# Performance work log

Hardware: AMD Instinct MI355X
Metric: run time of the kernel (lower is better)

## Reference

```python
import jax, jax.numpy as jnp
import numpy as np

B, T, W, R, N = 32, 256, 128, 4, 128
IFACE = R * W + 3 * W + 5 * R + 3   # 919
INSZ = (R + 1) * W                  # 640
DELTA = 1e-6

def _lstm_step(x, h, c, Wih, Whh, bih, bhh):
    g = x @ Wih.T + bih + h @ Whh.T + bhh
    i, f, gg, o = jnp.split(g, 4, axis=-1)
    c = jax.nn.sigmoid(f) * c + jax.nn.sigmoid(i) * jnp.tanh(gg)
    return jax.nn.sigmoid(o) * jnp.tanh(c), c

def _cosine(mem, keys):
    # mem [b,n,w], keys [b,h,w] -> [b,h,n]
    mn = mem / (jnp.linalg.norm(mem, axis=2, keepdims=True) + DELTA)
    kn = keys / (jnp.linalg.norm(keys, axis=2, keepdims=True) + DELTA)
    return jnp.einsum('bhw,bnw->bhn', kn, mn)

def _memory_step(xi, st):
    # xi: [b, IFACE] interface vector; st: DNC memory state
    mem, link, prec, rw, ww, usage = st
    b = xi.shape[0]
    o1 = R * W; o2 = o1 + R; o3 = o2 + W; o4 = o3 + 1
    o5 = o4 + W; o6 = o5 + W; o7 = o6 + R; o8 = o7 + 1; o9 = o8 + 1
    read_keys = jnp.tanh(xi[:, :o1].reshape(b, R, W))
    read_str = jax.nn.softplus(xi[:, o1:o2])
    write_key = jnp.tanh(xi[:, o2:o3])
    write_str = jax.nn.softplus(xi[:, o3:o4])
    erase = jax.nn.sigmoid(xi[:, o4:o5])
    write_vec = jnp.tanh(xi[:, o5:o6])
    free_gates = jax.nn.sigmoid(xi[:, o6:o7])
    alloc_gate = jax.nn.sigmoid(xi[:, o7:o8])
    write_gate = jax.nn.sigmoid(xi[:, o8:o9])
    read_modes = jax.nn.softmax(xi[:, o9:].reshape(b, R, 3), axis=-1)
    # usage vector update (single write head)
    usage = usage + (1 - usage) * ww
    usage = usage * jnp.prod(1 - free_gates[:, :, None] * rw, axis=1)
    # write content weighting [b,n]
    wc = jax.nn.softmax(_cosine(mem, write_key[:, None, :])[:, 0, :] * write_str, axis=1)
    # allocation weighting: sort ascending, exclusive cumprod, unsort
    u = DELTA + (1 - DELTA) * usage
    phi = jnp.argsort(u, axis=1)
    su = jnp.take_along_axis(u, phi, axis=1)
    prod_su = jnp.cumprod(jnp.concatenate([jnp.ones((b, 1), u.dtype), su], axis=1), axis=1)[:, :-1]
    alloc = jnp.take_along_axis((1 - su) * prod_su, jnp.argsort(phi, axis=1), axis=1)
    # write weighting [b,n]
    ww = write_gate * (alloc_gate * alloc + (1 - alloc_gate) * wc)
    # erase then write
    mem = mem * (1 - ww[:, :, None] * erase[:, None, :]) + ww[:, :, None] * write_vec[:, None, :]
    # temporal link matrix [b,n,n], zero diagonal
    link = (1 - ww[:, :, None] - ww[:, None, :]) * link + ww[:, :, None] * prec[:, None, :]
    link = link * (1 - jnp.eye(N, dtype=link.dtype))
    prec = (1 - jnp.sum(ww, axis=1, keepdims=True)) * prec + ww
    # read weighting: content + forward/backward temporal modes
    rc = jax.nn.softmax(_cosine(mem, read_keys) * read_str[:, :, None], axis=2)
    fw = jnp.einsum('bij,brj->bri', link, rw)
    bw = jnp.einsum('brj,bji->bri', rw, link)
    rw = read_modes[:, :, 0:1] * bw + read_modes[:, :, 1:2] * fw + read_modes[:, :, 2:3] * rc
    read_vecs = jnp.einsum('brn,bnw->bwr', rw, mem)  # [b,w,r] as used by controller
    return read_vecs, (mem, link, prec, rw, ww, usage)

def _forward(input, enc_Wih, enc_Whh, enc_bih, enc_bhh, ctl_Wih, ctl_Whh, ctl_bih, ctl_bhh, iface_W, iface_b, out_W, out_b):
    dt = input.dtype
    h0 = jnp.zeros((B, W), dt)
    def enc_step(carry, x_t):
        h, c = _lstm_step(x_t, carry[0], carry[1], enc_Wih, enc_Whh, enc_bih, enc_bhh)
        return (h, c), h
    _, enc = jax.lax.scan(enc_step, (h0, h0), jnp.swapaxes(input, 0, 1))  # enc: [T,B,W]
    z = lambda *s: jnp.zeros(s, dt)
    mem0 = (z(B, N, W), z(B, N, N), z(B, N), z(B, R, N), z(B, N), z(B, N))
    def step(carry, enc_t):
        h, c, rv, mst = carry
        # cat([b,w,1],[b,w,r]) then flatten -> interleaved per memory-cell element, as in torch
        x = jnp.concatenate([enc_t[:, :, None], rv], axis=2).reshape(B, INSZ)
        h, c = _lstm_step(x, h, c, ctl_Wih, ctl_Whh, ctl_bih, ctl_bhh)
        xi = h @ iface_W.T + iface_b
        rv, mst = _memory_step(xi, mst)
        out_t = jnp.concatenate([h, rv.reshape(B, W * R)], axis=1) @ out_W.T + out_b
        return (h, c, rv, mst), out_t
    _, outs = jax.lax.scan(step, (h0, h0, z(B, W, R), mem0), enc)
    return jnp.swapaxes(outs, 0, 1)  # [B,T,W]

def setup_inputs():
    key = jax.random.key(0)
    ks = jax.random.split(key, 8)
    p = lambda k, s: jax.random.normal(k, s, jnp.float32) * 0.05
    return {
        'input': jax.random.normal(ks[0], (B, T, W), jnp.float32),
        'source_lengths': jnp.full((B,), T, jnp.int32),
        'enc_Wih': p(ks[1], (4 * W, W)), 'enc_Whh': p(ks[2], (4 * W, W)),
        'enc_bih': jnp.zeros((4 * W,), jnp.float32), 'enc_bhh': jnp.zeros((4 * W,), jnp.float32),
        'ctl_Wih': p(ks[3], (4 * W, INSZ)), 'ctl_Whh': p(ks[4], (4 * W, W)),
        'ctl_bih': jnp.zeros((4 * W,), jnp.float32), 'ctl_bhh': jnp.zeros((4 * W,), jnp.float32),
        'iface_W': p(ks[5], (IFACE, W)), 'iface_b': jnp.zeros((IFACE,), jnp.float32),
        'out_W': p(ks[6], (W, INSZ)), 'out_b': jnp.zeros((W,), jnp.float32),
    }

def reference(input, source_lengths, enc_Wih, enc_Whh, enc_bih, enc_bhh, ctl_Wih, ctl_Whh, ctl_bih, ctl_bhh, iface_W, iface_b, out_W, out_b):
    # source_lengths are all == T (full-length sequences), so pack/pad is identity.
    return _forward(input, enc_Wih, enc_Whh, enc_bih, enc_bhh, ctl_Wih, ctl_Whh, ctl_bih, ctl_bhh, iface_W, iface_b, out_W, out_b)
```

## Files before the change

### kernel.cpp

```cpp
#include <hip/hip_runtime.h>

typedef unsigned short u16;
typedef unsigned int u32;

#define NT 1024
#define Bv 32
#define Tv 256
#define Wv 128
#define Rv 4
#define Nv 128
#define DELTAv 1e-6f

__device__ __forceinline__ float bf2f(u16 u){
  union { u32 i; float f; } c; c.i = ((u32)u) << 16; return c.f;
}
__device__ __forceinline__ u16 f2bf(float f){
  union { float f; u32 u; } c; c.f = f;
  u32 u = c.u;
  return (u16)((u + 0x7fffu + ((u >> 16) & 1u)) >> 16);
}
__device__ __forceinline__ void unp(u32 v, float& a, float& b){
  union { u32 i; float f; } c0, c1;
  c0.i = v << 16; c1.i = v & 0xffff0000u;
  a = c0.f; b = c1.f;
}
__device__ __forceinline__ float sigm(float x){ return 1.0f / (1.0f + __expf(-x)); }
__device__ __forceinline__ float softplusf(float x){ return fmaxf(x, 0.f) + log1pf(__expf(-fabsf(x))); }
__device__ __forceinline__ float wredsum(float v){
  #pragma unroll
  for (int o = 32; o > 0; o >>= 1) v += __shfl_down(v, o, 64);
  return v;
}
__device__ __forceinline__ float wredmax(float v){
  #pragma unroll
  for (int o = 32; o > 0; o >>= 1) v = fmaxf(v, __shfl_down(v, o, 64));
  return v;
}
__device__ __forceinline__ float ldval(const void* p, int idx, int dt32){
  return dt32 ? ((const float*)p)[idx] : bf2f(((const u16*)p)[idx]);
}

__global__ void detect_dtype(const u16* __restrict__ buf, int* __restrict__ flag){
  int lane = threadIdx.x;
  float crazy = 0.f;
  for (int i = 0; i < 4; i++){
    u16 v = buf[lane * 4 + i];
    int e = (v >> 7) & 0xFF;
    if (e != 0 && (e < 117 || e > 137)) crazy += 1.f;
  }
  crazy = wredsum(crazy);
  if (lane == 0) flag[0] = (crazy >= 32.f) ? 1 : 0;
}

__global__ void pack_w(const void* __restrict__ src, u32* __restrict__ dst,
                       int Js, int Jd, int K, const int* __restrict__ flag){
  int j = blockIdx.x * 256 + threadIdx.x;
  int k2 = blockIdx.y;
  if (j >= Jd) return;
  u16 lo = 0, hi = 0;
  if (j < Js){
    if (flag[0]){
      const float* s = (const float*)src;
      lo = f2bf(s[(size_t)j * K + 2 * k2]);
      hi = f2bf(s[(size_t)j * K + 2 * k2 + 1]);
    } else {
      const u16* s = (const u16*)src;
      lo = s[(size_t)j * K + 2 * k2];
      hi = s[(size_t)j * K + 2 * k2 + 1];
    }
  }
  dst[(size_t)k2 * Jd + j] = (u32)lo | ((u32)hi << 16);
}

__device__ __forceinline__ int permctl(int c){
  if (c < 128) return 5 * c;
  int q = c - 128; return 5 * (q & 127) + 1 + (q >> 7);
}
__device__ __forceinline__ int permout(int c){
  if (c < 128) return c;
  int q = c - 128; return 128 + 4 * (q & 127) + (q >> 7);
}

__global__ void pack_ctl(const void* __restrict__ src, u32* __restrict__ dst,
                         const int* __restrict__ flag){
  int j = blockIdx.x * 256 + threadIdx.x;
  int k2 = blockIdx.y;
  if (j >= 512) return;
  int c0 = permctl(2 * k2), c1 = permctl(2 * k2 + 1);
  u16 lo, hi;
  if (flag[0]){
    const float* s = (const float*)src;
    lo = f2bf(s[(size_t)j * 640 + c0]); hi = f2bf(s[(size_t)j * 640 + c1]);
  } else {
    const u16* s = (const u16*)src;
    lo = s[(size_t)j * 640 + c0]; hi = s[(size_t)j * 640 + c1];
  }
  dst[(size_t)k2 * 512 + j] = (u32)lo | ((u32)hi << 16);
}

__global__ void pack_out(const void* __restrict__ src, u32* __restrict__ dst,
                         const int* __restrict__ flag){
  int j = threadIdx.x;
  int k2 = blockIdx.y;
  if (j >= 128) return;
  int c0 = permout(2 * k2), c1 = permout(2 * k2 + 1);
  u16 lo, hi;
  if (flag[0]){
    const float* s = (const float*)src;
    lo = f2bf(s[(size_t)j * 640 + c0]); hi = f2bf(s[(size_t)j * 640 + c1]);
  } else {
    const u16* s = (const u16*)src;
    lo = s[(size_t)j * 640 + c0]; hi = s[(size_t)j * 640 + c1];
  }
  dst[(size_t)k2 * 128 + j] = (u32)lo | ((u32)hi << 16);
}

__global__ void fill_half(u16* __restrict__ p, int n){
  int i = blockIdx.x * 256 + threadIdx.x;
  if (i < n) p[i] = 0x3F00;
}

__global__ __launch_bounds__(NT) void dnc_main(
    const void* __restrict__ input,
    const void* __restrict__ enc_bih_g, const void* __restrict__ enc_bhh_g,
    const void* __restrict__ ctl_bih_g, const void* __restrict__ ctl_bhh_g,
    const void* __restrict__ iface_b_g, const void* __restrict__ out_b_g,
    const u32* __restrict__ encPW, const u32* __restrict__ ctlPW,
    const u32* __restrict__ ifPW, const u32* __restrict__ outPW,
    void* __restrict__ outp, const int* __restrict__ dtflag)
{
  const int bid = blockIdx.x;
  const int tid = threadIdx.x;
  const int lane = tid & 63;
  const int wid = tid >> 6;
  const int dt32 = dtflag[0];

  __shared__ __align__(16) float memS[Nv * 129];
  __shared__ __align__(16) float linkS[Nv * 129];
  __shared__ __align__(16) float pp[NT];
  __shared__ __align__(16) float ppE[512];
  __shared__ __align__(16) float xhC[768];
  __shared__ __align__(16) float xinS[128];
  __shared__ __align__(16) float rkeyS[512], rwS[512], rcS[512];
  __shared__ __align__(16) float wkeyS[128], eraseS[128], wvecS[128];
  __shared__ __align__(16) float wwS[128], usageS[128], precS[128], wcS[128];
  __shared__ __align__(16) float uS[128], sortedU[128], scanA[128];
  __shared__ __align__(16) float encBias[512], ctlBias[512];
  __shared__ __align__(16) float outBias[128];
  __shared__ float rstrS[4], fgS[4], rmRaw[12], rmS[12], scal[8];

  const int wE = (tid >= 919) ? (tid - 919) : (tid < 23 ? 105 + tid : -1);
  float cE = 0.f;
  float cC = 0.f;

  if (tid < 512){
    encBias[tid] = ldval(enc_bih_g, tid, dt32) + ldval(enc_bhh_g, tid, dt32);
    ctlBias[tid] = ldval(ctl_bih_g, tid, dt32) + ldval(ctl_bhh_g, tid, dt32);
    rwS[tid] = 0.f;
  }
  if (tid < 768) xhC[tid] = 0.f;
  if (tid < 128){
    outBias[tid] = ldval(out_b_g, tid, dt32);
    wwS[tid] = 0.f; usageS[tid] = 0.f; precS[tid] = 0.f;
  }
  for (int i = tid; i < Nv * 129; i += NT){ memS[i] = 0.f; linkS[i] = 0.f; }
  if (tid < 64){
    int idx = (bid * Tv + 0) * Wv + 2 * tid;
    xinS[2 * tid] = ldval(input, idx, dt32);
    xinS[2 * tid + 1] = ldval(input, idx + 1, dt32);
  }
  __syncthreads();

  if (tid >= 512){
    int o = tid - 512;
    const u32* wp = encPW + o;
    float a0 = 0.f, a1 = 0.f;
    #pragma unroll 8
    for (int k2 = 0; k2 < 64; k2++){
      float w0, w1; unp(wp[k2 * 512], w0, w1);
      float2 x2 = *(const float2*)(xinS + 2 * k2);
      a0 = fmaf(x2.x, w0, a0); a1 = fmaf(x2.y, w1, a1);
    }
    ppE[o] = a0 + a1;
  }
  __syncthreads();
  if (wE >= 0){
    float g0 = ppE[wE] + encBias[wE];
    float g1 = ppE[128 + wE] + encBias[128 + wE];
    float g2 = ppE[256 + wE] + encBias[256 + wE];
    float g3 = ppE[384 + wE] + encBias[384 + wE];
    float cn = sigm(g1) * cE + sigm(g0) * tanhf(g2);
    cE = cn;
    xhC[wE] = sigm(g3) * tanhf(cn);
  }
  if (tid >= 64 && tid < 128){
    int w2 = (tid - 64) * 2;
    int idx = (bid * Tv + 1) * Wv + w2;
    xinS[w2] = ldval(input, idx, dt32);
    xinS[w2 + 1] = ldval(input, idx + 1, dt32);
  }
  __syncthreads();

  for (int t = 0; t < Tv; ++t){
    {
      int o = tid & 511, s = tid >> 9;
      const u32* wp = ctlPW + (s * 192) * 512 + o;
      const float* xp = xhC + s * 384;
      float a0 = 0.f, a1 = 0.f;
      u32 wb[8];
      #pragma unroll
      for (int i = 0; i < 8; i++) wb[i] = wp[i * 512];
      #pragma unroll 1
      for (int c = 0; c < 184; c += 8){
        u32 wn[8];
        #pragma unroll
        for (int i = 0; i < 8; i++) wn[i] = wp[(c + 8 + i) * 512];
        #pragma unroll
        for (int i = 0; i < 8; i++){
          float w0, w1; unp(wb[i], w0, w1);
          float2 x2 = *(const float2*)(xp + 2 * (c + i));
          a0 = fmaf(x2.x, w0, a0); a1 = fmaf(x2.y, w1, a1);
          wb[i] = wn[i];
        }
      }
      #pragma unroll
      for (int i = 0; i < 8; i++){
        float w0, w1; unp(wb[i], w0, w1);
        float2 x2 = *(const float2*)(xp + 2 * (184 + i));
        a0 = fmaf(x2.x, w0, a0); a1 = fmaf(x2.y, w1, a1);
      }
      pp[tid] = a0 + a1;
    }
    __syncthreads();

    if (tid < 128){
      float g0 = pp[tid] + pp[512 + tid] + ctlBias[tid];
      float g1 = pp[128 + tid] + pp[640 + tid] + ctlBias[128 + tid];
      float g2 = pp[256 + tid] + pp[768 + tid] + ctlBias[256 + tid];
      float g3 = pp[384 + tid] + pp[896 + tid] + ctlBias[384 + tid];
      float cn = sigm(g1) * cC + sigm(g0) * tanhf(g2);
      cC = cn;
      xhC[640 + tid] = sigm(g3) * tanhf(cn);
    } else if (tid >= 512){
      int o = tid - 512;
      const u32* wp = encPW + o;
      float a0 = 0.f, a1 = 0.f;
      u32 wb[8];
      #pragma unroll
      for (int i = 0; i < 8; i++) wb[i] = wp[i * 512];
      #pragma unroll 1
      for (int c = 0; c < 56; c += 8){
        u32 wn[8];
        #pragma unroll
        for (int i = 0; i < 8; i++) wn[i] = wp[(c + 8 + i) * 512];
        #pragma unroll
        for (int i = 0; i < 8; i++){
          float w0, w1; unp(wb[i], w0, w1);
          float2 x2 = *(const float2*)(xinS + 2 * (c + i));
          a0 = fmaf(x2.x, w0, a0); a1 = fmaf(x2.y, w1, a1);
          wb[i] = wn[i];
        }
      }
      #pragma unroll
      for (int i = 0; i < 8; i++){
        float w0, w1; unp(wb[i], w0, w1);
        float2 x2 = *(const float2*)(xinS + 2 * (56 + i));
        a0 = fmaf(x2.x, w0, a0); a1 = fmaf(x2.y, w1, a1);
      }
      const u32* wq = encPW + 64 * 512 + o;
      #pragma unroll
      for (int i = 0; i < 8; i++) wb[i] = wq[i * 512];
      #pragma unroll 1
      for (int c = 0; c < 56; c += 8){
        u32 wn[8];
        #pragma unroll
        for (int i = 0; i < 8; i++) wn[i] = wq[(c + 8 + i) * 512];
        #pragma unroll
        for (int i = 0; i < 8; i++){
          float w0, w1; unp(wb[i], w0, w1);
          float2 x2 = *(const float2*)(xhC + 2 * (c + i));
          a0 = fmaf(x2.x, w0, a0); a1 = fmaf(x2.y, w1, a1);
          wb[i] = wn[i];
        }
      }
      #pragma unroll
      for (int i = 0; i < 8; i++){
        float w0, w1; unp(wb[i], w0, w1);
        float2 x2 = *(const float2*)(xhC + 2 * (56 + i));
        a0 = fmaf(x2.x, w0, a0); a1 = fmaf(x2.y, w1, a1);
      }
      ppE[o] = a0 + a1;
    }
    __syncthreads();

    if (tid < 919){
      const u32* wp = ifPW + tid;
      const float* xp = xhC + 640;
      float a0 = ldval(iface_b_g, tid, dt32), a1 = 0.f;
      u32 wb[8];
      #pragma unroll
      for (int i = 0; i < 8; i++) wb[i] = wp[i * 928];
      #pragma unroll 1
      for (int c = 0; c < 56; c += 8){
        u32 wn[8];
        #pragma unroll
        for (int i = 0; i < 8; i++) wn[i] = wp[(c + 8 + i) * 928];
        #pragma unroll
        for (int i = 0; i < 8; i++){
          float w0, w1; unp(wb[i], w0, w1);
          float2 x2 = *(const float2*)(xp + 2 * (c + i));
          a0 = fmaf(x2.x, w0, a0); a1 = fmaf(x2.y, w1, a1);
          wb[i] = wn[i];
        }
      }
      #pragma unroll
      for (int i = 0; i < 8; i++){
        float w0, w1; unp(wb[i], w0, w1);
        float2 x2 = *(const float2*)(xp + 2 * (56 + i));
        a0 = fmaf(x2.x, w0, a0); a1 = fmaf(x2.y, w1, a1);
      }
      pp[tid] = a0 + a1;
    }
    if (wE >= 0){
      float g0 = ppE[wE] + encBias[wE];
      float g1 = ppE[128 + wE] + encBias[128 + wE];
      float g2 = ppE[256 + wE] + encBias[256 + wE];
      float g3 = ppE[384 + wE] + encBias[384 + wE];
      float cn = sigm(g1) * cE + sigm(g0) * tanhf(g2);
      cE = cn;
      xhC[wE] = sigm(g3) * tanhf(cn);
    }
    __syncthreads();

    if (tid < 919){
      float v = pp[tid];
      if (tid < 512) rkeyS[tid] = tanhf(v);
      else if (tid < 516) rstrS[tid - 512] = softplusf(v);
      else if (tid < 644) wkeyS[tid - 516] = tanhf(v);
      else if (tid == 644) scal[0] = softplusf(v);
      else if (tid < 773) eraseS[tid - 645] = sigm(v);
      else if (tid < 901) wvecS[tid - 773] = tanhf(v);
      else if (tid < 905) fgS[tid - 901] = sigm(v);
      else if (tid == 905) scal[1] = sigm(v);
      else if (tid == 906) scal[2] = sigm(v);
      else rmRaw[tid - 907] = v;
    } else if (tid >= 928 && tid < 992){
      int w2 = (tid - 928) * 2;
      int col = (t + 2 < Tv) ? t + 2 : Tv - 1;
      int idx = (bid * Tv + col) * Wv + w2;
      xinS[w2] = ldval(input, idx, dt32);
      xinS[w2 + 1] = ldval(input, idx + 1, dt32);
    }
    __syncthreads();

    if (wid < 5){
      float* arr = (wid < 4) ? (rkeyS + wid * 128) : wkeyS;
      float a = arr[lane], bq = arr[lane + 64];
      float s = wredsum(a * a + bq * bq);
      s = __shfl(s, 0, 64);
      float inv = 1.0f / (sqrtf(s) + DELTAv);
      arr[lane] = a * inv; arr[lane + 64] = bq * inv;
    } else if (wid < 7){
      int n = (wid - 5) * 64 + lane;
      float us = usageS[n];
      us = us + (1.f - us) * wwS[n];
      float ret = (1.f - fgS[0] * rwS[n]) * (1.f - fgS[1] * rwS[128 + n]) *
                  (1.f - fgS[2] * rwS[256 + n]) * (1.f - fgS[3] * rwS[384 + n]);
      usageS[n] = us * ret;
    } else if (tid >= 448 && tid < 452){
      int r = tid - 448;
      float m0 = rmRaw[3 * r], m1 = rmRaw[3 * r + 1], m2 = rmRaw[3 * r + 2];
      float mx = fmaxf(m0, fmaxf(m1, m2));
      float e0 = __expf(m0 - mx), e1 = __expf(m1 - mx), e2 = __expf(m2 - mx);
      float s = e0 + e1 + e2;
      rmS[3 * r] = e0 / s; rmS[3 * r + 1] = e1 / s; rmS[3 * r + 2] = e2 / s;
    }
    __syncthreads();

    if (tid < 128){
      float sq = 0.f, dt = 0.f;
      #pragma unroll 8
      for (int j = 0; j < 128; j++){
        float m = memS[tid * 129 + j];
        sq = fmaf(m, m, sq); dt = fmaf(m, wkeyS[j], dt);
      }
      wcS[tid] = dt / (sqrtf(sq) + DELTAv) * scal[0];
    } else if (tid < 256){
      uS[tid - 128] = DELTAv + (1.f - DELTAv) * usageS[tid - 128];
    }
    __syncthreads();

    int rnk = 0;
    if (wid == 0){
      float a = wcS[lane], bq = wcS[lane + 64];
      float mx = wredmax(fmaxf(a, bq)); mx = __shfl(mx, 0, 64);
      float ea = __expf(a - mx), eb = __expf(bq - mx);
      float s = wredsum(ea + eb); s = __shfl(s, 0, 64);
      wcS[lane] = ea / s; wcS[lane + 64] = eb / s;
    } else if (tid >= 64 && tid < 192){
      int n = tid - 64;
      float un = uS[n];
      int r = 0;
      for (int m = 0; m < 128; m++){
        float um = uS[m];
        r += (um < un) || (um == un && m < n);
      }
      rnk = r;
      sortedU[r] = un;
    }
    __syncthreads();

    if (wid == 8){
      float a = sortedU[2 * lane], bq = sortedU[2 * lane + 1];
      float p = a * bq;
      float incl = p;
      #pragma unroll
      for (int o = 1; o < 64; o <<= 1){
        float tv = __shfl_up(incl, o, 64);
        if (lane >= o) incl *= tv;
      }
      float ex = __shfl_up(incl, 1, 64);
      if (lane == 0) ex = 1.f;
      scanA[2 * lane] = ex * a;
      scanA[2 * lane + 1] = ex * p;
    }
    __syncthreads();

    if (tid >= 64 && tid < 192){
      int n = tid - 64;
      float ex = (rnk == 0) ? 1.f : scanA[rnk - 1];
      float al = (1.f - uS[n]) * ex;
      wwS[n] = scal[2] * (scal[1] * al + (1.f - scal[1]) * wcS[n]);
    }
    __syncthreads();

    if (wid == 0){
      float s = wredsum(wwS[lane] + wwS[64 + lane]);
      if (lane == 0) scal[3] = s;
    }
    __syncthreads();

    #pragma unroll
    for (int it = 0; it < 16; it++){
      int e = it * NT + tid;
      int n = e >> 7, w = e & 127;
      float wwn = wwS[n];
      float m = memS[n * 129 + w];
      memS[n * 129 + w] = m * (1.f - wwn * eraseS[w]) + wwn * wvecS[w];
      float l = linkS[n * 129 + w];
      linkS[n * 129 + w] = (n == w) ? 0.f
        : ((1.f - wwn - wwS[w]) * l + wwn * precS[w]);
    }
    __syncthreads();

    if (tid < 128){
      float sq = 0.f, d0 = 0.f, d1 = 0.f, d2 = 0.f, d3 = 0.f;
      #pragma unroll 4
      for (int j = 0; j < 128; j++){
        float m = memS[tid * 129 + j];
        sq = fmaf(m, m, sq);
        d0 = fmaf(m, rkeyS[j], d0);
        d1 = fmaf(m, rkeyS[128 + j], d1);
        d2 = fmaf(m, rkeyS[256 + j], d2);
        d3 = fmaf(m, rkeyS[384 + j], d3);
      }
      float inv = 1.f / (sqrtf(sq) + DELTAv);
      rcS[tid]       = d0 * inv * rstrS[0];
      rcS[128 + tid] = d1 * inv * rstrS[1];
      rcS[256 + tid] = d2 * inv * rstrS[2];
      rcS[384 + tid] = d3 * inv * rstrS[3];
    } else if (tid < 256){
      int n = tid - 128;
      precS[n] = (1.f - scal[3]) * precS[n] + wwS[n];
    }
    __syncthreads();

    if (wid < 4){
      float a = rcS[wid * 128 + lane], bq = rcS[wid * 128 + 64 + lane];
      float mx = wredmax(fmaxf(a, bq)); mx = __shfl(mx, 0, 64);
      float ea = __expf(a - mx), eb = __expf(bq - mx);
      float s = wredsum(ea + eb); s = __shfl(s, 0, 64);
      rcS[wid * 128 + lane] = ea / s; rcS[wid * 128 + 64 + lane] = eb / s;
    }
    __syncthreads();

    if (tid < 512){
      int r = tid >> 7, i = tid & 127;
      const float* rwp = rwS + r * 128;
      float acc = 0.f;
      #pragma unroll 8
      for (int j = 0; j < 128; j++) acc = fmaf(rwp[j], linkS[i * 129 + j], acc);
      pp[tid] = acc;
    } else {
      int o = tid - 512; int r = o >> 7, i = o & 127;
      const float* rwp = rwS + r * 128;
      float acc = 0.f;
      #pragma unroll 8
      for (int j = 0; j < 128; j++) acc = fmaf(rwp[j], linkS[j * 129 + i], acc);
      pp[tid] = acc;
    }
    __syncthreads();

    if (tid < 512){
      int r = tid >> 7;
      rwS[tid] = rmS[3 * r] * pp[512 + tid] + rmS[3 * r + 1] * pp[tid] + rmS[3 * r + 2] * rcS[tid];
    }
    __syncthreads();

    {
      int s = tid >> 9, o = tid & 511, r = o >> 7, w = o & 127;
      float acc = 0.f;
      #pragma unroll 8
      for (int q = 0; q < 64; q++){
        int n = s * 64 + q;
        acc = fmaf(rwS[r * 128 + n], memS[n * 129 + w], acc);
      }
      pp[tid] = acc;
    }
    __syncthreads();

    if (tid < 512) xhC[128 + tid] = pp[tid] + pp[512 + tid];
    __syncthreads();

    {
      int s8 = tid >> 7, j = tid & 127;
      const u32* wp = outPW + (s8 * 40) * 128 + j;
      float a0 = 0.f, a1 = 0.f;
      #pragma unroll 8
      for (int q = 0; q < 40; q++){
        int k2 = s8 * 40 + q;
        const float* xb = (k2 < 64) ? (xhC + 640 + 2 * k2) : (xhC + 2 * k2);
        float w0, w1; unp(wp[q * 128], w0, w1);
        a0 = fmaf(xb[0], w0, a0); a1 = fmaf(xb[1], w1, a1);
      }
      pp[tid] = a0 + a1;
    }
    __syncthreads();

    if (tid < 128){
      float o = outBias[tid];
      #pragma unroll
      for (int s = 0; s < 8; s++) o += pp[s * 128 + tid];
      size_t oi = ((size_t)bid * Tv + t) * Wv + tid;
      if (dt32) ((float*)outp)[oi] = o;
      else ((u16*)outp)[oi] = f2bf(o);
    }
    __syncthreads();
  }
}

extern "C" void kernel_launch(void* const* d_in, const int* in_sizes, int n_in,
                              void* d_out, int out_size, void* d_ws, size_t ws_size,
                              hipStream_t stream) {
  (void)in_sizes; (void)n_in;
  const void* input   = d_in[0];
  const void* enc_Wih = d_in[2];
  const void* enc_Whh = d_in[3];
  const void* enc_bih = d_in[4];
  const void* enc_bhh = d_in[5];
  const void* ctl_Wih = d_in[6];
  const void* ctl_Whh = d_in[7];
  const void* ctl_bih = d_in[8];
  const void* ctl_bhh = d_in[9];
  const void* iface_W = d_in[10];
  const void* iface_b = d_in[11];
  const void* out_W   = d_in[12];
  const void* out_b   = d_in[13];

  char* ws = (char*)d_ws;
  size_t off = 0;
  int* dtflag = (int*)(ws + off); off += 256;
  u32* encPW  = (u32*)(ws + off); off += (size_t)128 * 512 * 4;
  u32* ctlPW  = (u32*)(ws + off); off += (size_t)384 * 512 * 4;
  u32* ifPW   = (u32*)(ws + off); off += (size_t)64 * 928 * 4;
  u32* outPW  = (u32*)(ws + off); off += (size_t)320 * 128 * 4;
  const size_t need_bytes = off;

  if (ws_size < need_bytes){
    fill_half<<<dim3((out_size + 255) / 256), dim3(256), 0, stream>>>((u16*)d_out, out_size);
    return;
  }

  detect_dtype<<<dim3(1), dim3(64), 0, stream>>>((const u16*)input, dtflag);

  pack_w<<<dim3(2, 64), 256, 0, stream>>>(enc_Wih, encPW, 512, 512, 128, dtflag);
  pack_w<<<dim3(2, 64), 256, 0, stream>>>(enc_Whh, encPW + 64 * 512, 512, 512, 128, dtflag);
  pack_ctl<<<dim3(2, 320), 256, 0, stream>>>(ctl_Wih, ctlPW, dtflag);
  pack_w<<<dim3(2, 64), 256, 0, stream>>>(ctl_Whh, ctlPW + 320 * 512, 512, 512, 128, dtflag);
  pack_w<<<dim3(4, 64), 256, 0, stream>>>(iface_W, ifPW, 919, 928, 128, dtflag);
  pack_out<<<dim3(1, 320), 128, 0, stream>>>(out_W, outPW, dtflag);

  dnc_main<<<dim3(Bv), dim3(NT), 0, stream>>>(
      input, enc_bih, enc_bhh, ctl_bih, ctl_bhh, iface_b, out_b,
      encPW, ctlPW, ifPW, outPW, d_out, dtflag);
}
```

Measured before the change: 11.21 ms.

## Store weights as fp32 pairs, packed-FMA gemv helper, merge DNC step phases

Weights are now packed as float2 (fp32) rather than bf16 pairs, and a templated gemv helper uses packed two-wide vector FMAs, removing the unpack shifts. Several per-step phases are merged to cut barriers: the memory-norm pass overlaps with the usage update, sort, scan and allocation run in one wavefront, the link products overlap with precedence, and the read-weight softmax fuses with the mode mix. The output projection is split so part of it overlaps the read-vector computation, and the output write is deferred to the next step. This doubles weight memory traffic and changes precision from bf16 to fp32 weights.

```diff
diff --git a/kernel.cpp b/kernel.cpp
--- a/kernel.cpp
+++ b/kernel.cpp
@@ -2,6 +2,7 @@
 
 typedef unsigned short u16;
 typedef unsigned int u32;
+typedef float v2f __attribute__((ext_vector_type(2)));
 
 #define NT 1024
 #define Bv 32
@@ -19,11 +20,6 @@
   u32 u = c.u;
   return (u16)((u + 0x7fffu + ((u >> 16) & 1u)) >> 16);
 }
-__device__ __forceinline__ void unp(u32 v, float& a, float& b){
-  union { u32 i; float f; } c0, c1;
-  c0.i = v << 16; c1.i = v & 0xffff0000u;
-  a = c0.f; b = c1.f;
-}
 __device__ __forceinline__ float sigm(float x){ return 1.0f / (1.0f + __expf(-x)); }
 __device__ __forceinline__ float softplusf(float x){ return fmaxf(x, 0.f) + log1pf(__expf(-fabsf(x))); }
 __device__ __forceinline__ float wredsum(float v){
@@ -38,6 +34,31 @@
 }
 __device__ __forceinline__ float ldval(const void* p, int idx, int dt32){
   return dt32 ? ((const float*)p)[idx] : bf2f(((const u16*)p)[idx]);
+}
+
+template<int ITERS, int STRIDE>
+__device__ __forceinline__ float gemv_f2(const float2* __restrict__ wp, const float* __restrict__ xp){
+  v2f acc = (v2f)(0.f);
+  v2f wb[8], wn[8];
+  #pragma unroll
+  for (int i = 0; i < 8; i++){ float2 t = wp[i * STRIDE]; wb[i] = (v2f){t.x, t.y}; }
+  #pragma unroll 1
+  for (int c = 0; c < ITERS - 8; c += 8){
+    #pragma unroll
+    for (int i = 0; i < 8; i++){ float2 t = wp[(c + 8 + i) * STRIDE]; wn[i] = (v2f){t.x, t.y}; }
+    #pragma unroll
+    for (int i = 0; i < 8; i++){
+      v2f x2 = *(const v2f*)(xp + 2 * (c + i));
+      acc += wb[i] * x2;
+      wb[i] = wn[i];
+    }
+  }
+  #pragma unroll
+  for (int i = 0; i < 8; i++){
+    v2f x2 = *(const v2f*)(xp + 2 * (ITERS - 8 + i));
+    acc += wb[i] * x2;
+  }
+  return acc.x + acc.y;
 }
 
 __global__ void detect_dtype(const u16* __restrict__ buf, int* __restrict__ flag){
@@ -52,24 +73,21 @@
   if (lane == 0) flag[0] = (crazy >= 32.f) ? 1 : 0;
 }
 
-__global__ void pack_w(const void* __restrict__ src, u32* __restrict__ dst,
+__device__ __forceinline__ float rdsrc(const void* s, size_t idx, int f32){
+  return f32 ? ((const float*)s)[idx] : bf2f(((const u16*)s)[idx]);
+}
+
+__global__ void pack_w(const void* __restrict__ src, float2* __restrict__ dst,
                        int Js, int Jd, int K, const int* __restrict__ flag){
   int j = blockIdx.x * 256 + threadIdx.x;
   int k2 = blockIdx.y;
   if (j >= Jd) return;
-  u16 lo = 0, hi = 0;
+  float2 o = make_float2(0.f, 0.f);
   if (j < Js){
-    if (flag[0]){
-      const float* s = (const float*)src;
-      lo = f2bf(s[(size_t)j * K + 2 * k2]);
-      hi = f2bf(s[(size_t)j * K + 2 * k2 + 1]);
-    } else {
-      const u16* s = (const u16*)src;
-      lo = s[(size_t)j * K + 2 * k2];
-      hi = s[(size_t)j * K + 2 * k2 + 1];
-    }
-  }
-  dst[(size_t)k2 * Jd + j] = (u32)lo | ((u32)hi << 16);
+    o.x = rdsrc(src, (size_t)j * K + 2 * k2, flag[0]);
+    o.y = rdsrc(src, (size_t)j * K + 2 * k2 + 1, flag[0]);
+  }
+  dst[(size_t)k2 * Jd + j] = o;
 }
 
 __device__ __forceinline__ int permctl(int c){
@@ -81,38 +99,26 @@
   int q = c - 128; return 128 + 4 * (q & 127) + (q >> 7);
 }
 
-__global__ void pack_ctl(const void* __restrict__ src, u32* __restrict__ dst,
+__global__ void pack_ctl(const void* __restrict__ src, float2* __restrict__ dst,
                          const int* __restrict__ flag){
   int j = blockIdx.x * 256 + threadIdx.x;
   int k2 = blockIdx.y;
   if (j >= 512) return;
-  int c0 = permctl(2 * k2), c1 = permctl(2 * k2 + 1);
-  u16 lo, hi;
-  if (flag[0]){
-    const float* s = (const float*)src;
-    lo = f2bf(s[(size_t)j * 640 + c0]); hi = f2bf(s[(size_t)j * 640 + c1]);
-  } else {
-    const u16* s = (const u16*)src;
-    lo = s[(size_t)j * 640 + c0]; hi = s[(size_t)j * 640 + c1];
-  }
-  dst[(size_t)k2 * 512 + j] = (u32)lo | ((u32)hi << 16);
-}
-
-__global__ void pack_out(const void* __restrict__ src, u32* __restrict__ dst,
+  float2 o;
+  o.x = rdsrc(src, (size_t)j * 640 + permctl(2 * k2), flag[0]);
+  o.y = rdsrc(src, (size_t)j * 640 + permctl(2 * k2 + 1), flag[0]);
+  dst[(size_t)k2 * 512 + j] = o;
+}
+
+__global__ void pack_out(const void* __restrict__ src, float2* __restrict__ dst,
                          const int* __restrict__ flag){
   int j = threadIdx.x;
   int k2 = blockIdx.y;
   if (j >= 128) return;
-  int c0 = permout(2 * k2), c1 = permout(2 * k2 + 1);
-  u16 lo, hi;
-  if (flag[0]){
-    const float* s = (const float*)src;
-    lo = f2bf(s[(size_t)j * 640 + c0]); hi = f2bf(s[(size_t)j * 640 + c1]);
-  } else {
-    const u16* s = (const u16*)src;
-    lo = s[(size_t)j * 640 + c0]; hi = s[(size_t)j * 640 + c1];
-  }
-  dst[(size_t)k2 * 128 + j] = (u32)lo | ((u32)hi << 16);
+  float2 o;
+  o.x = rdsrc(src, (size_t)j * 640 + permout(2 * k2), flag[0]);
+  o.y = rdsrc(src, (size_t)j * 640 + permout(2 * k2 + 1), flag[0]);
+  dst[(size_t)k2 * 128 + j] = o;
 }
 
 __global__ void fill_half(u16* __restrict__ p, int n){
@@ -125,8 +131,8 @@
     const void* __restrict__ enc_bih_g, const void* __restrict__ enc_bhh_g,
     const void* __restrict__ ctl_bih_g, const void* __restrict__ ctl_bhh_g,
     const void* __restrict__ iface_b_g, const void* __restrict__ out_b_g,
-    const u32* __restrict__ encPW, const u32* __restrict__ ctlPW,
-    const u32* __restrict__ ifPW, const u32* __restrict__ outPW,
+    const float2* __restrict__ encPW, const float2* __restrict__ ctlPW,
+    const float2* __restrict__ ifPW, const float2* __restrict__ outPW,
     void* __restrict__ outp, const int* __restrict__ dtflag)
 {
   const int bid = blockIdx.x;
@@ -138,13 +144,13 @@
   __shared__ __align__(16) float memS[Nv * 129];
   __shared__ __align__(16) float linkS[Nv * 129];
   __shared__ __align__(16) float pp[NT];
-  __shared__ __align__(16) float ppE[512];
+  __shared__ __align__(16) float ppE[NT];
   __shared__ __align__(16) float xhC[768];
   __shared__ __align__(16) float xinS[128];
   __shared__ __align__(16) float rkeyS[512], rwS[512], rcS[512];
   __shared__ __align__(16) float wkeyS[128], eraseS[128], wvecS[128];
   __shared__ __align__(16) float wwS[128], usageS[128], precS[128], wcS[128];
-  __shared__ __align__(16) float uS[128], sortedU[128], scanA[128];
+  __shared__ __align__(16) float uS[128], sortedU[128], scanA[128], alS[128], sqS[128];
   __shared__ __align__(16) float encBias[512], ctlBias[512];
   __shared__ __align__(16) float outBias[128];
   __shared__ float rstrS[4], fgS[4], rmRaw[12], rmS[12], scal[8];
@@ -173,15 +179,7 @@
 
   if (tid >= 512){
     int o = tid - 512;
-    const u32* wp = encPW + o;
-    float a0 = 0.f, a1 = 0.f;
-    #pragma unroll 8
-    for (int k2 = 0; k2 < 64; k2++){
-      float w0, w1; unp(wp[k2 * 512], w0, w1);
-      float2 x2 = *(const float2*)(xinS + 2 * k2);
-      a0 = fmaf(x2.x, w0, a0); a1 = fmaf(x2.y, w1, a1);
-    }
-    ppE[o] = a0 + a1;
+    ppE[o] = gemv_f2<64, 512>(encPW + o, xinS);
   }
   __syncthreads();
   if (wE >= 0){
@@ -202,34 +200,17 @@
   __syncthreads();
 
   for (int t = 0; t < Tv; ++t){
+    if (t > 0 && tid < 128){
+      float o = outBias[tid];
+      #pragma unroll
+      for (int s = 0; s < 8; s++) o += ppE[s * 128 + tid];
+      size_t oi = ((size_t)bid * Tv + (t - 1)) * Wv + tid;
+      if (dt32) ((float*)outp)[oi] = o;
+      else ((u16*)outp)[oi] = f2bf(o);
+    }
     {
-      int o = tid & 511, s = tid >> 9;
-      const u32* wp = ctlPW + (s * 192) * 512 + o;
-      const float* xp = xhC + s * 384;
-      float a0 = 0.f, a1 = 0.f;
-      u32 wb[8];
-      #pragma unroll
-      for (int i = 0; i < 8; i++) wb[i] = wp[i * 512];
-      #pragma unroll 1
-      for (int c = 0; c < 184; c += 8){
-        u32 wn[8];
-        #pragma unroll
-        for (int i = 0; i < 8; i++) wn[i] = wp[(c + 8 + i) * 512];
-        #pragma unroll
-        for (int i = 0; i < 8; i++){
-          float w0, w1; unp(wb[i], w0, w1);
-          float2 x2 = *(const float2*)(xp + 2 * (c + i));
-          a0 = fmaf(x2.x, w0, a0); a1 = fmaf(x2.y, w1, a1);
-          wb[i] = wn[i];
-        }
-      }
-      #pragma unroll
-      for (int i = 0; i < 8; i++){
-        float w0, w1; unp(wb[i], w0, w1);
-        float2 x2 = *(const float2*)(xp + 2 * (184 + i));
-        a0 = fmaf(x2.x, w0, a0); a1 = fmaf(x2.y, w1, a1);
-      }
-      pp[tid] = a0 + a1;
+      int s = tid >> 9, o = tid & 511;
+      pp[tid] = gemv_f2<192, 512>(ctlPW + (s * 192) * 512 + o, xhC + s * 384);
     }
     __syncthreads();
 
@@ -243,83 +224,13 @@
       xhC[640 + tid] = sigm(g3) * tanhf(cn);
     } else if (tid >= 512){
       int o = tid - 512;
-      const u32* wp = encPW + o;
-      float a0 = 0.f, a1 = 0.f;
-      u32 wb[8];
-      #pragma unroll
-      for (int i = 0; i < 8; i++) wb[i] = wp[i * 512];
-      #pragma unroll 1
-      for (int c = 0; c < 56; c += 8){
-        u32 wn[8];
-        #pragma unroll
-        for (int i = 0; i < 8; i++) wn[i] = wp[(c + 8 + i) * 512];
-        #pragma unroll
-        for (int i = 0; i < 8; i++){
-          float w0, w1; unp(wb[i], w0, w1);
-          float2 x2 = *(const float2*)(xinS + 2 * (c + i));
-          a0 = fmaf(x2.x, w0, a0); a1 = fmaf(x2.y, w1, a1);
-          wb[i] = wn[i];
-        }
-      }
-      #pragma unroll
-      for (int i = 0; i < 8; i++){
-        float w0, w1; unp(wb[i], w0, w1);
-        float2 x2 = *(const float2*)(xinS + 2 * (56 + i));
-        a0 = fmaf(x2.x, w0, a0); a1 = fmaf(x2.y, w1, a1);
-      }
-      const u32* wq = encPW + 64 * 512 + o;
-      #pragma unroll
-      for (int i = 0; i < 8; i++) wb[i] = wq[i * 512];
-      #pragma unroll 1
-      for (int c = 0; c < 56; c += 8){
-        u32 wn[8];
-        #pragma unroll
-        for (int i = 0; i < 8; i++) wn[i] = wq[(c + 8 + i) * 512];
-        #pragma unroll
-        for (int i = 0; i < 8; i++){
-          float w0, w1; unp(wb[i], w0, w1);
-          float2 x2 = *(const float2*)(xhC + 2 * (c + i));
-          a0 = fmaf(x2.x, w0, a0); a1 = fmaf(x2.y, w1, a1);
-          wb[i] = wn[i];
-        }
-      }
-      #pragma unroll
-      for (int i = 0; i < 8; i++){
-        float w0, w1; unp(wb[i], w0, w1);
-        float2 x2 = *(const float2*)(xhC + 2 * (56 + i));
-        a0 = fmaf(x2.x, w0, a0); a1 = fmaf(x2.y, w1, a1);
-      }
-      ppE[o] = a0 + a1;
+      ppE[o] = gemv_f2<64, 512>(encPW + o, xinS)
+             + gemv_f2<64, 512>(encPW + 64 * 512 + o, xhC);
     }
     __syncthreads();
 
     if (tid < 919){
-      const u32* wp = ifPW + tid;
-      const float* xp = xhC + 640;
-      float a0 = ldval(iface_b_g, tid, dt32), a1 = 0.f;
-      u32 wb[8];
-      #pragma unroll
-      for (int i = 0; i < 8; i++) wb[i] = wp[i * 928];
-      #pragma unroll 1
-      for (int c = 0; c < 56; c += 8){
-        u32 wn[8];
-        #pragma unroll
-        for (int i = 0; i < 8; i++) wn[i] = wp[(c + 8 + i) * 928];
-        #pragma unroll
-        for (int i = 0; i < 8; i++){
-          float w0, w1; unp(wb[i], w0, w1);
-          float2 x2 = *(const float2*)(xp + 2 * (c + i));
-          a0 = fmaf(x2.x, w0, a0); a1 = fmaf(x2.y, w1, a1);
-          wb[i] = wn[i];
-        }
-      }
-      #pragma unroll
-      for (int i = 0; i < 8; i++){
-        float w0, w1; unp(wb[i], w0, w1);
-        float2 x2 = *(const float2*)(xp + 2 * (56 + i));
-        a0 = fmaf(x2.x, w0, a0); a1 = fmaf(x2.y, w1, a1);
-      }
-      pp[tid] = a0 + a1;
+      pp[tid] = ldval(iface_b_g, tid, dt32) + gemv_f2<64, 928>(ifPW + tid, xhC + 640);
     }
     if (wE >= 0){
       float g0 = ppE[wE] + encBias[wE];
@@ -366,7 +277,9 @@
       us = us + (1.f - us) * wwS[n];
       float ret = (1.f - fgS[0] * rwS[n]) * (1.f - fgS[1] * rwS[128 + n]) *
                   (1.f - fgS[2] * rwS[256 + n]) * (1.f - fgS[3] * rwS[384 + n]);
-      usageS[n] = us * ret;
+      us *= ret;
+      usageS[n] = us;
+      uS[n] = DELTAv + (1.f - DELTAv) * us;
     } else if (tid >= 448 && tid < 452){
       int r = tid - 448;
       float m0 = rmRaw[3 * r], m1 = rmRaw[3 * r + 1], m2 = rmRaw[3 * r + 2];
@@ -374,68 +287,65 @@
       float e0 = __expf(m0 - mx), e1 = __expf(m1 - mx), e2 = __expf(m2 - mx);
       float s = e0 + e1 + e2;
       rmS[3 * r] = e0 / s; rmS[3 * r + 1] = e1 / s; rmS[3 * r + 2] = e2 / s;
-    }
-    __syncthreads();
-
-    if (tid < 128){
-      float sq = 0.f, dt = 0.f;
+    } else if (wid >= 8 && wid < 10){
+      int n = (wid - 8) * 64 + lane;
+      float sq = 0.f;
       #pragma unroll 8
       for (int j = 0; j < 128; j++){
-        float m = memS[tid * 129 + j];
-        sq = fmaf(m, m, sq); dt = fmaf(m, wkeyS[j], dt);
+        float m = memS[n * 129 + j];
+        sq = fmaf(m, m, sq);
       }
-      wcS[tid] = dt / (sqrtf(sq) + DELTAv) * scal[0];
-    } else if (tid < 256){
-      uS[tid - 128] = DELTAv + (1.f - DELTAv) * usageS[tid - 128];
-    }
-    __syncthreads();
-
-    int rnk = 0;
+      sqS[n] = sq;
+    }
+    __syncthreads();
+
+    if (tid < 128){
+      float dt = 0.f;
+      #pragma unroll 8
+      for (int j = 0; j < 128; j++) dt = fmaf(memS[tid * 129 + j], wkeyS[j], dt);
+      wcS[tid] = dt / (sqrtf(sqS[tid]) + DELTAv) * scal[0];
+    }
+    __syncthreads();
+
     if (wid == 0){
       float a = wcS[lane], bq = wcS[lane + 64];
       float mx = wredmax(fmaxf(a, bq)); mx = __shfl(mx, 0, 64);
       float ea = __expf(a - mx), eb = __expf(bq - mx);
       float s = wredsum(ea + eb); s = __shfl(s, 0, 64);
       wcS[lane] = ea / s; wcS[lane + 64] = eb / s;
-    } else if (tid >= 64 && tid < 192){
-      int n = tid - 64;
-      float un = uS[n];
-      int r = 0;
+    } else if (wid == 1){
+      int l = lane;
+      float u0 = uS[l], u1 = uS[64 + l];
+      int r0 = 0, r1 = 0;
       for (int m = 0; m < 128; m++){
         float um = uS[m];
-        r += (um < un) || (um == un && m < n);
+        r0 += (um < u0) || (um == u0 && m < l);
+        r1 += (um < u1) || (um == u1 && m < 64 + l);
       }
-      rnk = r;
-      sortedU[r] = un;
-    }
-    __syncthreads();
-
-    if (wid == 8){
-      float a = sortedU[2 * lane], bq = sortedU[2 * lane + 1];
+      sortedU[r0] = u0; sortedU[r1] = u1;
+      float a = sortedU[2 * l], bq = sortedU[2 * l + 1];
       float p = a * bq;
       float incl = p;
       #pragma unroll
       for (int o = 1; o < 64; o <<= 1){
         float tv = __shfl_up(incl, o, 64);
-        if (lane >= o) incl *= tv;
+        if (l >= o) incl *= tv;
       }
-      float ex = __shfl_up(incl, 1, 64);
-      if (lane == 0) ex = 1.f;
-      scanA[2 * lane] = ex * a;
-      scanA[2 * lane + 1] = ex * p;
-    }
-    __syncthreads();
-
-    if (tid >= 64 && tid < 192){
-      int n = tid - 64;
-      float ex = (rnk == 0) ? 1.f : scanA[rnk - 1];
-      float al = (1.f - uS[n]) * ex;
-      wwS[n] = scal[2] * (scal[1] * al + (1.f - scal[1]) * wcS[n]);
+      float exh = __shfl_up(incl, 1, 64);
+      if (l == 0) exh = 1.f;
+      scanA[2 * l] = exh;
+      scanA[2 * l + 1] = exh * a;
+      float ex0 = scanA[r0], ex1 = scanA[r1];
+      alS[l] = (1.f - u0) * ex0;
+      alS[64 + l] = (1.f - u1) * ex1;
     }
     __syncthreads();
 
     if (wid == 0){
-      float s = wredsum(wwS[lane] + wwS[64 + lane]);
+      float w0v = scal[2] * (scal[1] * alS[lane] + (1.f - scal[1]) * wcS[lane]);
+      float w1v = scal[2] * (scal[1] * alS[64 + lane] + (1.f - scal[1]) * wcS[64 + lane]);
+      wwS[lane] = w0v; wwS[64 + lane] = w1v;
+      float s = wredsum(w0v + w1v);
       if (lane == 0) scal[3] = s;
     }
     __syncthreads();
@@ -472,80 +382,70 @@
     } else if (tid < 256){
       int n = tid - 128;
       precS[n] = (1.f - scal[3]) * precS[n] + wwS[n];
-    }
-    __syncthreads();
-
-    if (wid < 4){
-      float a = rcS[wid * 128 + lane], bq = rcS[wid * 128 + 64 + lane];
-      float mx = wredmax(fmaxf(a, bq)); mx = __shfl(mx, 0, 64);
-      float ea = __expf(a - mx), eb = __expf(bq - mx);
-      float s = wredsum(ea + eb); s = __shfl(s, 0, 64);
-      rcS[wid * 128 + lane] = ea / s; rcS[wid * 128 + 64 + lane] = eb / s;
-    }
-    __syncthreads();
-
-    if (tid < 512){
-      int r = tid >> 7, i = tid & 127;
+    } else if (tid < 768){
+      int o = tid - 256, r = o >> 7, i = o & 127;
       const float* rwp = rwS + r * 128;
       float acc = 0.f;
       #pragma unroll 8
       for (int j = 0; j < 128; j++) acc = fmaf(rwp[j], linkS[i * 129 + j], acc);
-      pp[tid] = acc;
+      pp[o] = acc;
     } else {
-      int o = tid - 512; int r = o >> 7, i = o & 127;
+      int o2 = tid - 768, i = o2 & 127;
+      int r1 = o2 >> 7, r2 = r1 + 2;
+      const float* rw1 = rwS + r1 * 128;
+      const float* rw2 = rwS + r2 * 128;
+      float accA = 0.f, accB = 0.f;
+      #pragma unroll 8
+      for (int j = 0; j < 128; j++){
+        float l = linkS[j * 129 + i];
+        accA = fmaf(rw1[j], l, accA);
+        accB = fmaf(rw2[j], l, accB);
+      }
+      pp[512 + o2] = accA;
+      pp[512 + o2 + 256] = accB;
+    }
+    __syncthreads();
+
+    if (wid < 4){
+      int r = wid;
+      float a = rcS[r * 128 + lane], bq = rcS[r * 128 + 64 + lane];
+      float mx = wredmax(fmaxf(a, bq)); mx = __shfl(mx, 0, 64);
+      float ea = __expf(a - mx), eb = __expf(bq - mx);
+      float s = wredsum(ea + eb); s = __shfl(s, 0, 64);
+      float pa = ea / s, pb = eb / s;
+      int o0 = r * 128 + lane, o1 = o0 + 64;
+      rwS[o0] = rmS[3 * r] * pp[512 + o0] + rmS[3 * r + 1] * pp[o0] + rmS[3 * r + 2] * pa;
+      rwS[o1] = rmS[3 * r] * pp[512 + o1] + rmS[3 * r + 1] * pp[o1] + rmS[3 * r + 2] * pb;
+    }
+    __syncthreads();
+
+    if (tid < 512){
+      int r = tid >> 7, w = tid & 127;
       const float* rwp = rwS + r * 128;
       float acc = 0.f;
       #pragma unroll 8
-      for (int j = 0; j < 128; j++) acc = fmaf(rwp[j], linkS[j * 129 + i], acc);
-      pp[tid] = acc;
+      for (int n = 0; n < 128; n++) acc = fmaf(rwp[n], memS[n * 129 + w], acc);
+      xhC[128 + tid] = acc;
+    } else {
+      int s = (tid - 512) >> 7, j = tid & 127;
+      ppE[tid] = gemv_f2<16, 128>(outPW + (s * 16) * 128 + j, xhC + 640 + 32 * s);
     }
     __syncthreads();
 
     if (tid < 512){
-      int r = tid >> 7;
-      rwS[tid] = rmS[3 * r] * pp[512 + tid] + rmS[3 * r + 1] * pp[tid] + rmS[3 * r + 2] * rcS[tid];
-    }
-    __syncthreads();
-
-    {
-      int s = tid >> 9, o = tid & 511, r = o >> 7, w = o & 127;
-      float acc = 0.f;
-      #pragma unroll 8
-      for (int q = 0; q < 64; q++){
-        int n = s * 64 + q;
-        acc = fmaf(rwS[r * 128 + n], memS[n * 129 + w], acc);
-      }
-      pp[tid] = acc;
-    }
-    __syncthreads();
-
-    if (tid < 512) xhC[128 + tid] = pp[tid] + pp[512 + tid];
-    __syncthreads();
-
-    {
-      int s8 = tid >> 7, j = tid & 127;
-      const u32* wp = outPW + (s8 * 40) * 128 + j;
-      float a0 = 0.f, a1 = 0.f;
-      #pragma unroll 8
-      for (int q = 0; q < 40; q++){
-        int k2 = s8 * 40 + q;
-        const float* xb = (k2 < 64) ? (xhC + 640 + 2 * k2) : (xhC + 2 * k2);
-        float w0, w1; unp(wp[q * 128], w0, w1);
-        a0 = fmaf(xb[0], w0, a0); a1 = fmaf(xb[1], w1, a1);
-      }
-      pp[tid] = a0 + a1;
-    }
-    __syncthreads();
-
-    if (tid < 128){
-      float o = outBias[tid];
-      #pragma unroll
-      for (int s = 0; s < 8; s++) o += pp[s * 128 + tid];
-      size_t oi = ((size_t)bid * Tv + t) * Wv + tid;
-      if (dt32) ((float*)outp)[oi] = o;
-      else ((u16*)outp)[oi] = f2bf(o);
-    }
-    __syncthreads();
+      int s = tid >> 7, j = tid & 127;
+      ppE[tid] = gemv_f2<64, 128>(outPW + (64 + s * 64) * 128 + j, xhC + 128 + 128 * s);
+    }
+    __syncthreads();
+  }
+
+  if (tid < 128){
+    float o = outBias[tid];
+    #pragma unroll
+    for (int s = 0; s < 8; s++) o += ppE[s * 128 + tid];
+    size_t oi = ((size_t)bid * Tv + (Tv - 1)) * Wv + tid;
+    if (dt32) ((float*)outp)[oi] = o;
+    else ((u16*)outp)[oi] = f2bf(o);
   }
 }
 
@@ -570,10 +470,10 @@
   char* ws = (char*)d_ws;
   size_t off = 0;
   int* dtflag = (int*)(ws + off); off += 256;
-  u32* encPW  = (u32*)(ws + off); off += (size_t)128 * 512 * 4;
-  u32* ctlPW  = (u32*)(ws + off); off += (size_t)384 * 512 * 4;
-  u32* ifPW   = (u32*)(ws + off); off += (size_t)64 * 928 * 4;
-  u32* outPW  = (u32*)(ws + off); off += (size_t)320 * 128 * 4;
+  float2* encPW = (float2*)(ws + off); off += (size_t)128 * 512 * 8;
+  float2* ctlPW = (float2*)(ws + off); off += (size_t)384 * 512 * 8;
+  float2* ifPW  = (float2*)(ws + off); off += (size_t)64 * 928 * 8;
+  float2* outPW = (float2*)(ws + off); off += (size_t)320 * 128 * 8;
   const size_t need_bytes = off;
 
   if (ws_size < need_bytes){
```

Result: slower. 20.09 ms (+79.2%).
